# Kernel tuning notes

Measured on AMD Instinct MI355X. Metric: run time of the kernel, lower is better.

Reference implementation:

```python
import jax, jax.numpy as jnp
import numpy as np

H, W = 512, 512
STRIDE = 4
SCALE_RATIO = 32.0
POST_MIN = 2.0
POST_MAX = 100.0
BG_RATIO = 0.15
CUT_OFF = 100.0


def setup_inputs() -> dict:
    key = jax.random.key(0)
    k1, k2, k3, k4 = jax.random.split(key, 4)
    B, N = 8, 256
    scale = jax.random.uniform(k1, (B, N, 2), dtype=jnp.float32)          # raw scales in [0,1)
    rotation = jax.random.normal(k2, (B, N, 1), dtype=jnp.float32)        # rotation angle per point
    points = jax.random.uniform(k3, (B, N, 2), dtype=jnp.float32,
                                minval=0.0, maxval=float(W))              # head coords in image
    st_sizes = jax.random.uniform(k4, (B,), dtype=jnp.float32,
                                  minval=256.0, maxval=512.0)             # unused in math (as in torch)
    return {"scale": scale, "rotation": rotation, "points": points, "st_sizes": st_sizes}


def reference(scale, rotation, points, st_sizes):
    # grid centers, meshgrid indexing='xy' -> (H/stride, W/stride)
    xx = jnp.arange(0, W, STRIDE, dtype=jnp.float32) + STRIDE / 2
    yy = jnp.arange(0, H, STRIDE, dtype=jnp.float32) + STRIDE / 2
    gx, gy = jnp.meshgrid(xx, yy, indexing='xy')
    gx = gx.reshape(-1)   # (HW,)
    gy = gy.reshape(-1)

    # per-point anisotropic scales, clamped as in torch
    s = jnp.clip(SCALE_RATIO * scale, STRIDE / POST_MIN, POST_MAX)        # (B,N,2)
    sx2 = s[..., 0] ** 2                                                  # (B,N)
    sy2 = s[..., 1] ** 2

    th = rotation[..., 0]
    c, si = jnp.cos(th), jnp.sin(th)
    # covariance = R diag(sx2, sy2) R^T  (2x2 symmetric, closed form)
    cov_a = c * c * sx2 + si * si * sy2
    cov_b = c * si * (sx2 - sy2)
    cov_d = si * si * sx2 + c * c * sy2
    det = sx2 * sy2                                                       # det(cov), (B,N)
    inv_a = cov_d / det
    inv_b = -cov_b / det
    inv_d = cov_a / det

    # displacement from each grid center to each point: (B,N,HW)
    dx = gx[None, None, :] - points[..., 0:1]
    dy = gy[None, None, :] - points[..., 1:2]

    # z = -0.5 * xy^T inv_cov xy
    z = -0.5 * (inv_a[..., None] * dx * dx
                + 2.0 * inv_b[..., None] * dx * dy
                + inv_d[..., None] * dy * dy)                             # (B,N,HW)

    likelihood = z - 0.5 * jnp.log(det)[..., None]

    # background likelihood (use_bg and cut_off set)
    min_z = jnp.max(z, axis=1)                                            # (B,HW)
    idx = jnp.argmax(z, axis=1)                                           # (B,HW)
    d_const = -0.5 * CUT_OFF * CUT_OFF
    bk_z = d_const - min_z
    det_sel = jnp.take_along_axis(det, idx, axis=1)                       # (B,HW)
    bk_like = bk_z - jnp.log(det_sel / BG_RATIO)

    likelihood = jnp.concatenate([likelihood, bk_like[:, None, :]], axis=1)  # (B,N+1,HW)
    return jax.nn.softmax(likelihood, axis=1)
```

## Files before the change

kernel.cpp:

```cpp
#include <hip/hip_runtime.h>


#define HWC 16384
#define NPTS 256
#define NBATCH 8

__global__ __launch_bounds__(256) void post_prob_kernel(
    const float* __restrict__ scale,
    const float* __restrict__ rotation,
    const float* __restrict__ points,
    float* __restrict__ out)
{
    __shared__ float sA[NPTS];
    __shared__ float sB[NPTS];
    __shared__ float sD[NPTS];
    __shared__ float sHL[NPTS];
    __shared__ float sLD[NPTS];
    __shared__ float sPX[NPTS];
    __shared__ float sPY[NPTS];

    const int b  = blockIdx.x >> 6;
    const int hw = ((blockIdx.x & 63) << 8) + threadIdx.x;

    {
        const int n = threadIdx.x;
        const int base = (b * NPTS + n);
        float sx = scale[base * 2 + 0];
        float sy = scale[base * 2 + 1];
        sx = fminf(fmaxf(32.0f * sx, 2.0f), 100.0f);
        sy = fminf(fmaxf(32.0f * sy, 2.0f), 100.0f);
        float sx2 = sx * sx, sy2 = sy * sy;
        float th = rotation[base];
        float c, si;
        __sincosf(th, &si, &c);
        float cov_a = c * c * sx2 + si * si * sy2;
        float cov_b = c * si * (sx2 - sy2);
        float cov_d = si * si * sx2 + c * c * sy2;
        float det   = sx2 * sy2;
        float rdet  = 1.0f / det;
        float inv_a = cov_d * rdet;
        float inv_b = -cov_b * rdet;
        float inv_d = cov_a * rdet;
        float logdet = logf(det);
        sA[n]  = -0.5f * inv_a;
        sB[n]  = -inv_b;
        sD[n]  = -0.5f * inv_d;
        sHL[n] = -0.5f * logdet;
        sLD[n] = logdet;
        sPX[n] = points[base * 2 + 0];
        sPY[n] = points[base * 2 + 1];
    }
    __syncthreads();

    const float gx = (float)((hw & 127) * 4 + 2);
    const float gy = (float)((hw >> 7) * 4 + 2);

    float m      = -INFINITY;
    float best_z = -INFINITY;
    int   best_n = 0;
    #pragma unroll 4
    for (int n = 0; n < NPTS; ++n) {
        float dx = gx - sPX[n];
        float dy = gy - sPY[n];
        float z  = sA[n] * dx * dx + sB[n] * (dx * dy) + sD[n] * dy * dy;
        float like = z + sHL[n];
        m = fmaxf(m, like);
        if (z > best_z) { best_z = z; best_n = n; }
    }
    const float LOG_BG = -1.8971199848858813f;
    const float bk = -5000.0f - best_z - sLD[best_n] + LOG_BG;
    m = fmaxf(m, bk);

    float sum = 0.0f;
    #pragma unroll 4
    for (int n = 0; n < NPTS; ++n) {
        float dx = gx - sPX[n];
        float dy = gy - sPY[n];
        float z  = sA[n] * dx * dx + sB[n] * (dx * dy) + sD[n] * dy * dy;
        sum += __expf(z + sHL[n] - m);
    }
    sum += __expf(bk - m);
    const float inv = 1.0f / sum;

    float* __restrict__ outb = out + (size_t)b * 257 * HWC + hw;
    #pragma unroll 4
    for (int n = 0; n < NPTS; ++n) {
        float dx = gx - sPX[n];
        float dy = gy - sPY[n];
        float z  = sA[n] * dx * dx + sB[n] * (dx * dy) + sD[n] * dy * dy;
        outb[(size_t)n * HWC] = __expf(z + sHL[n] - m) * inv;
    }
    outb[(size_t)256 * HWC] = __expf(bk - m) * inv;
}

extern "C" void kernel_launch(void* const* d_in, const int* in_sizes, int n_in,
                              void* d_out, int out_size, void* d_ws, size_t ws_size,
                              hipStream_t stream) {
    const float* scale    = (const float*)d_in[0];
    const float* rotation = (const float*)d_in[1];
    const float* points   = (const float*)d_in[2];
    float* out = (float*)d_out;
    (void)in_sizes; (void)n_in; (void)out_size; (void)d_ws; (void)ws_size;

    dim3 grid(NBATCH * (HWC / 256));
    dim3 block(256);
    post_prob_kernel<<<grid, block, 0, stream>>>(scale, rotation, points, out);
}
```

Measured before the change: 166.1 us.

## Precompute expanded quadratic coefficients in prep kernel and use base-2 softmax

A separate prep kernel computes per-point coefficients once, expanding the quadratic form into a polynomial in gx, gy with log2e folded in. Those coefficients go to workspace as float4 pairs. The main kernel reads them with uniform global loads instead of building shared memory in every block. It evaluates each likelihood with a chain of FMAs, uses exp2f, and folds the normalisation into the exponent so the multiply by the reciprocal goes away. The cost is an extra launch, possible precision loss from expanding the polynomial at large coordinates, and reliance on scalar/cache loads rather than LDS.

```diff
diff --git a/kernel.cpp b/kernel.cpp
--- a/kernel.cpp
+++ b/kernel.cpp
@@ -5,92 +5,102 @@
 #define NPTS 256
 #define NBATCH 8
 
-__global__ __launch_bounds__(256) void post_prob_kernel(
+#define K_LOG2E 1.4426950408889634f
+#define BK_CONST (-7216.2121700389835f)
+
+__global__ __launch_bounds__(256) void prep_kernel(
     const float* __restrict__ scale,
     const float* __restrict__ rotation,
     const float* __restrict__ points,
+    float4* __restrict__ P)
+{
+    const int i = blockIdx.x * 256 + threadIdx.x;
+    if (i >= NBATCH * NPTS) return;
+
+    float sx = fminf(fmaxf(32.0f * scale[i * 2 + 0], 2.0f), 100.0f);
+    float sy = fminf(fmaxf(32.0f * scale[i * 2 + 1], 2.0f), 100.0f);
+    float sx2 = sx * sx, sy2 = sy * sy;
+
+    float th = rotation[i];
+    float s, c;
+    sincosf(th, &s, &c);
+    float cov_a = c * c * sx2 + s * s * sy2;
+    float cov_b = c * s * (sx2 - sy2);
+    float cov_d = s * s * sx2 + c * c * sy2;
+    float det  = sx2 * sy2;
+    float rdet = 1.0f / det;
+
+    float KA = -0.5f * K_LOG2E * (cov_d * rdet);
+    float KB =         K_LOG2E * (cov_b * rdet);
+    float KD = -0.5f * K_LOG2E * (cov_a * rdet);
+
+    float px = points[i * 2 + 0];
+    float py = points[i * 2 + 1];
+
+    float cx = -(2.0f * KA * px + KB * py);
+    float cy = -(KB * px + 2.0f * KD * py);
+    float cz = KA * px * px + KB * px * py + KD * py * py;
+
+    float l2det = log2f(det);
+    float HLK = -0.5f * l2det;
+
+    P[i * 2 + 0] = make_float4(KA, KB, KD, cx);
+    P[i * 2 + 1] = make_float4(cy, cz + HLK, HLK, l2det);
+}
+
+__global__ __launch_bounds__(256) void post_prob_kernel(
+    const float4* __restrict__ P,
     float* __restrict__ out)
 {
-    __shared__ float sA[NPTS];
-    __shared__ float sB[NPTS];
-    __shared__ float sD[NPTS];
-    __shared__ float sHL[NPTS];
-    __shared__ float sLD[NPTS];
-    __shared__ float sPX[NPTS];
-    __shared__ float sPY[NPTS];
-
     const int b  = blockIdx.x >> 6;
     const int hw = ((blockIdx.x & 63) << 8) + threadIdx.x;
 
-    {
-        const int n = threadIdx.x;
-        const int base = (b * NPTS + n);
-        float sx = scale[base * 2 + 0];
-        float sy = scale[base * 2 + 1];
-        sx = fminf(fmaxf(32.0f * sx, 2.0f), 100.0f);
-        sy = fminf(fmaxf(32.0f * sy, 2.0f), 100.0f);
-        float sx2 = sx * sx, sy2 = sy * sy;
-        float th = rotation[base];
-        float c, si;
-        __sincosf(th, &si, &c);
-        float cov_a = c * c * sx2 + si * si * sy2;
-        float cov_b = c * si * (sx2 - sy2);
-        float cov_d = si * si * sx2 + c * c * sy2;
-        float det   = sx2 * sy2;
-        float rdet  = 1.0f / det;
-        float inv_a = cov_d * rdet;
-        float inv_b = -cov_b * rdet;
-        float inv_d = cov_a * rdet;
-        float logdet = logf(det);
-        sA[n]  = -0.5f * inv_a;
-        sB[n]  = -inv_b;
-        sD[n]  = -0.5f * inv_d;
-        sHL[n] = -0.5f * logdet;
-        sLD[n] = logdet;
-        sPX[n] = points[base * 2 + 0];
-        sPY[n] = points[base * 2 + 1];
-    }
-    __syncthreads();
-
     const float gx = (float)((hw & 127) * 4 + 2);
     const float gy = (float)((hw >> 7) * 4 + 2);
+    const float gxx = gx * gx, gxy = gx * gy, gyy = gy * gy;
 
-    float m      = -INFINITY;
-    float best_z = -INFINITY;
-    int   best_n = 0;
-    #pragma unroll 4
+    const float4* __restrict__ Pb = P + (size_t)b * NPTS * 2;
+
+    float m   = -INFINITY;
+    float bz  = -INFINITY;
+    float bld = 0.0f;
+    #pragma unroll 8
     for (int n = 0; n < NPTS; ++n) {
-        float dx = gx - sPX[n];
-        float dy = gy - sPY[n];
-        float z  = sA[n] * dx * dx + sB[n] * (dx * dy) + sD[n] * dy * dy;
-        float like = z + sHL[n];
+        float4 q0 = Pb[n * 2 + 0];
+        float4 q1 = Pb[n * 2 + 1];
+        float like = fmaf(q0.x, gxx, fmaf(q0.y, gxy, fmaf(q0.z, gyy,
+                     fmaf(q0.w, gx,  fmaf(q1.x, gy, q1.y)))));
+        float z = like - q1.z;
         m = fmaxf(m, like);
-        if (z > best_z) { best_z = z; best_n = n; }
+        bool gt = z > bz;
+        bz  = gt ? z    : bz;
+        bld = gt ? q1.w : bld;
     }
-    const float LOG_BG = -1.8971199848858813f;
-    const float bk = -5000.0f - best_z - sLD[best_n] + LOG_BG;
+    const float bk = BK_CONST - bz - bld;
     m = fmaxf(m, bk);
 
     float sum = 0.0f;
-    #pragma unroll 4
+    #pragma unroll 8
     for (int n = 0; n < NPTS; ++n) {
-        float dx = gx - sPX[n];
-        float dy = gy - sPY[n];
-        float z  = sA[n] * dx * dx + sB[n] * (dx * dy) + sD[n] * dy * dy;
-        sum += __expf(z + sHL[n] - m);
+        float4 q0 = Pb[n * 2 + 0];
+        float4 q1 = Pb[n * 2 + 1];
+        float like = fmaf(q0.x, gxx, fmaf(q0.y, gxy, fmaf(q0.z, gyy,
+                     fmaf(q0.w, gx,  fmaf(q1.x, gy, q1.y)))));
+        sum += exp2f(like - m);
     }
-    sum += __expf(bk - m);
-    const float inv = 1.0f / sum;
+    sum += exp2f(bk - m);
+    const float m2 = m + log2f(sum);
 
     float* __restrict__ outb = out + (size_t)b * 257 * HWC + hw;
-    #pragma unroll 4
+    #pragma unroll 8
     for (int n = 0; n < NPTS; ++n) {
-        float dx = gx - sPX[n];
-        float dy = gy - sPY[n];
-        float z  = sA[n] * dx * dx + sB[n] * (dx * dy) + sD[n] * dy * dy;
-        outb[(size_t)n * HWC] = __expf(z + sHL[n] - m) * inv;
+        float4 q0 = Pb[n * 2 + 0];
+        float4 q1 = Pb[n * 2 + 1];
+        float like = fmaf(q0.x, gxx, fmaf(q0.y, gxy, fmaf(q0.z, gyy,
+                     fmaf(q0.w, gx,  fmaf(q1.x, gy, q1.y)))));
+        outb[(size_t)n * HWC] = exp2f(like - m2);
     }
-    outb[(size_t)256 * HWC] = __expf(bk - m) * inv;
+    outb[(size_t)256 * HWC] = exp2f(bk - m2);
 }
 
 extern "C" void kernel_launch(void* const* d_in, const int* in_sizes, int n_in,
@@ -100,9 +110,9 @@
     const float* rotation = (const float*)d_in[1];
     const float* points   = (const float*)d_in[2];
     float* out = (float*)d_out;
-    (void)in_sizes; (void)n_in; (void)out_size; (void)d_ws; (void)ws_size;
+    float4* P  = (float4*)d_ws;
+    (void)in_sizes; (void)n_in; (void)out_size; (void)ws_size;
 
-    dim3 grid(NBATCH * (HWC / 256));
-    dim3 block(256);
-    post_prob_kernel<<<grid, block, 0, stream>>>(scale, rotation, points, out);
+    prep_kernel<<<dim3(NBATCH), dim3(256), 0, stream>>>(scale, rotation, points, P);
+    post_prob_kernel<<<dim3(NBATCH * (HWC / 256)), dim3(256), 0, stream>>>(P, out);
 }
```

Result: slower. 193.0 us (+16.2%).
